# Performance work log

Measured on AMD Instinct MI355X. Metric: run time of the kernel, lower is better.

## Reference

```python
import jax, jax.numpy as jnp
import numpy as np

T = 2048        # q_len (current chunk)
P = 2048        # past KV cache length
HID = 4096      # hidden_size
H = 32          # num_attention_heads
D = HID // H    # head_dim = 128
THETA = 10000.0


def apply_rope(x, pos):
    # x: [H, T, D], pos: [T] int
    half = D // 2
    inv_freq = 1.0 / (THETA ** (jnp.arange(0, half, dtype=jnp.float32) / half))
    ang = pos.astype(jnp.float32)[:, None] * inv_freq[None, :]      # [T, D/2]
    cos = jnp.concatenate([jnp.cos(ang), jnp.cos(ang)], axis=-1)[None]  # [1, T, D]
    sin = jnp.concatenate([jnp.sin(ang), jnp.sin(ang)], axis=-1)[None]
    rot = jnp.concatenate([-x[..., half:], x[..., :half]], axis=-1)
    return x * cos + rot * sin


def setup_inputs() -> dict:
    key = jax.random.key(0)
    ks = jax.random.split(key, 8)
    s = 1.0 / np.sqrt(HID)
    inp = {
        "hidden_states": jax.random.normal(ks[0], (T, HID), dtype=jnp.float32),
        "attention_mask": jnp.triu(jnp.full((T, T), -jnp.inf, dtype=jnp.float32), k=1),
        "Wq": jax.random.normal(ks[1], (HID, HID), dtype=jnp.float32) * s,
        "Wk": jax.random.normal(ks[2], (HID, HID), dtype=jnp.float32) * s,
        "Wv": jax.random.normal(ks[3], (HID, HID), dtype=jnp.float32) * s,
        "Wo": jax.random.normal(ks[4], (HID, HID), dtype=jnp.float32) * s,
        "past_k": jax.random.normal(ks[5], (H, P, D), dtype=jnp.float32),
        "past_v": jax.random.normal(ks[6], (H, P, D), dtype=jnp.float32),
        "position_ids": P + jnp.arange(T, dtype=jnp.int32),
        "past_length": P,
    }
    return inp


def reference(hidden_states, attention_mask, Wq, Wk, Wv, Wo, past_k, past_v,
              position_ids, past_length):
    # QKV projections -> [H, T, D]
    proj = lambda W: (hidden_states @ W).reshape(T, H, D).transpose(1, 0, 2)
    q, k, v = proj(Wq), proj(Wk), proj(Wv)
    q = apply_rope(q, position_ids)
    k = apply_rope(k, position_ids)

    scale = 1.0 / jnp.sqrt(jnp.float32(D))
    # scores against past cache and current chunk (fp32 softmax, as in source)
    past_dots = (jnp.einsum('htd,hsd->hts', q, past_k) * scale).astype(jnp.float32)
    pmask = jnp.where(jnp.arange(P) < past_length, 0.0, -jnp.inf)  # [P]
    past_dots = past_dots + pmask
    cur = ((jnp.einsum('htd,hsd->hts', q, k) * scale) + attention_mask).astype(jnp.float32)

    # online-softmax merge via logsumexp combination
    past_lse = jax.scipy.special.logsumexp(past_dots, axis=-1, keepdims=True)
    cur_lse = jax.scipy.special.logsumexp(cur, axis=-1, keepdims=True)
    tot_lse = jnp.logaddexp(past_lse, cur_lse)
    pw = jnp.exp(past_dots - tot_lse).astype(q.dtype)
    cw = jnp.exp(cur - tot_lse).astype(q.dtype)

    out = jnp.einsum('hts,hsd->htd', pw, past_v) + jnp.einsum('hts,hsd->htd', cw, v)
    out = jnp.where(past_length == 0,
                    jnp.einsum('hts,hsd->htd', jax.nn.softmax(cur, axis=-1).astype(q.dtype), v),
                    out)
    out = out.transpose(1, 0, 2).reshape(T, HID)   # [T, hidden]
    return out @ Wo
```

## Files before the change

kernel.cpp:

```cpp
#include <hip/hip_runtime.h>
#include <cstdint>
#include <cstddef>

#define T_LEN 2048
#define PAST_MAX 2048
#define HID 4096
#define NHEAD 32
#define DHEAD 128

typedef __bf16 bf16_t;
typedef __bf16 bf16x4 __attribute__((ext_vector_type(4)));
typedef __bf16 bf16x8 __attribute__((ext_vector_type(8)));
typedef float  f32x4  __attribute__((ext_vector_type(4)));
typedef float  f32x16 __attribute__((ext_vector_type(16)));
typedef unsigned int u32x4 __attribute__((ext_vector_type(4)));

__device__ __forceinline__ void gload16(const void* g, void* l){
  __builtin_amdgcn_global_load_lds((const __attribute__((address_space(1))) void*)g,
                                   (__attribute__((address_space(3))) void*)l,
                                   16, 0, 0);
}

__device__ __forceinline__ unsigned pack_bf16(float a, float b){
  const unsigned ua = __builtin_bit_cast(unsigned short, (bf16_t)a);
  const unsigned ub = __builtin_bit_cast(unsigned short, (bf16_t)b);
  return ua | (ub << 16);
}

__global__ void cvt2_k(const float* __restrict__ a, bf16_t* __restrict__ ao,
                       const float* __restrict__ b, bf16_t* __restrict__ bo, int n4){
  int i = blockIdx.x * 256 + threadIdx.x;
  if (i < n4){
    const float4 v = ((const float4*)a)[i];
    bf16x4 o = { (bf16_t)v.x, (bf16_t)v.y, (bf16_t)v.z, (bf16_t)v.w };
    ((bf16x4*)ao)[i] = o;
  } else {
    i -= n4;
    const float4 v = ((const float4*)b)[i];
    bf16x4 o = { (bf16_t)v.x, (bf16_t)v.y, (bf16_t)v.z, (bf16_t)v.w };
    ((bf16x4*)bo)[i] = o;
  }
}

__global__ __launch_bounds__(256) void transpose2_k(const float* __restrict__ in,
                                                    bf16_t* __restrict__ out, int R, int C){
  __shared__ float tile[64][65];
  const int r0 = blockIdx.x << 6, c0 = blockIdx.y << 6;
  const size_t bo = (size_t)blockIdx.z * (size_t)R * (size_t)C;
  const int tx = threadIdx.x & 15, ty = threadIdx.x >> 4;
#pragma unroll
  for (int k = 0; k < 4; ++k){
    const float4 v = *(const float4*)(in + bo + (size_t)(r0 + ty + 16*k) * C + c0 + tx*4);
    float* tp = &tile[ty + 16*k][tx*4];
    tp[0] = v.x; tp[1] = v.y; tp[2] = v.z; tp[3] = v.w;
  }
  __syncthreads();
  const int rr0 = (threadIdx.x & 7) * 8;
  const int ccb = threadIdx.x >> 3;
#pragma unroll
  for (int k = 0; k < 2; ++k){
    const int cc = ccb + 32*k;
    bf16x8 o;
#pragma unroll
    for (int j = 0; j < 8; ++j) o[j] = (bf16_t)tile[rr0 + j][cc];
    *(bf16x8*)(out + bo + (size_t)(c0 + cc) * R + r0 + rr0) = o;
  }
}

__global__ __launch_bounds__(256) void transpose3_k(
    const float* __restrict__ s0, const float* __restrict__ s1, const float* __restrict__ s2,
    bf16_t* __restrict__ d0, bf16_t* __restrict__ d1, bf16_t* __restrict__ d2){
  __shared__ float tile[64][65];
  const float* in = (blockIdx.z == 0) ? s0 : (blockIdx.z == 1) ? s1 : s2;
  bf16_t* out = (blockIdx.z == 0) ? d0 : (blockIdx.z == 1) ? d1 : d2;
  const int r0 = blockIdx.x << 6, c0 = blockIdx.y << 6;
  const int tx = threadIdx.x & 15, ty = threadIdx.x >> 4;
#pragma unroll
  for (int k = 0; k < 4; ++k){
    const float4 v = *(const float4*)(in + (size_t)(r0 + ty + 16*k) * HID + c0 + tx*4);
    float* tp = &tile[ty + 16*k][tx*4];
    tp[0] = v.x; tp[1] = v.y; tp[2] = v.z; tp[3] = v.w;
  }
  __syncthreads();
  const int rr0 = (threadIdx.x & 7) * 8;
  const int ccb = threadIdx.x >> 3;
#pragma unroll
  for (int k = 0; k < 2; ++k){
    const int cc = ccb + 32*k;
    bf16x8 o;
#pragma unroll
    for (int j = 0; j < 8; ++j) o[j] = (bf16_t)tile[rr0 + j][cc];
    *(bf16x8*)(out + (size_t)(c0 + cc) * HID + r0 + rr0) = o;
  }
}

__global__ void ropek_k(bf16_t* __restrict__ K, const int* __restrict__ pos){
  const int idx = blockIdx.x * 256 + threadIdx.x;
  const int i = idx & 63;
  const int t = (idx >> 6) & (T_LEN - 1);
  const int h = idx >> 17;
  const size_t base = ((size_t)h * T_LEN + t) * DHEAD;
  const float p = (float)pos[t];
  const float inv = __expf(-(float)i * 0.14391156605212898f);
  const float ang = p * inv;
  float sn, cs;
  sincosf(ang, &sn, &cs);
  const float b0 = (float)K[base + i], b1 = (float)K[base + i + 64];
  K[base + i]      = (bf16_t)(b0 * cs - b1 * sn);
  K[base + i + 64] = (bf16_t)(b1 * cs + b0 * sn);
}

__global__ __launch_bounds__(512, 1) void gemmqkv8p_k(
    const bf16_t* __restrict__ A,
    const bf16_t* __restrict__ B0, const bf16_t* __restrict__ B1, const bf16_t* __restrict__ B2,
    bf16_t* __restrict__ OQ, bf16_t* __restrict__ OK2, bf16_t* __restrict__ OVT, int cpx)
{
  const int bid = blockIdx.x;
  const int wg  = (bid & 7) * cpx + (bid >> 3);
  const int mt  = wg & 7;
  const int nt  = wg >> 3;
  const int z   = nt >> 4;
  const int m0  = mt << 8;
  const int n0  = (nt & 15) << 8;
  const bf16_t* __restrict__ B = (z == 0) ? B0 : (z == 1) ? B1 : B2;

  const int tid = threadIdx.x;
  const int wv = tid >> 6, lane = tid & 63, lm = lane & 15, g = lane >> 4;
  const int wr = wv >> 2, wc = wv & 3;

  __shared__ __align__(16) char smem[131072];

  const f32x4 fzero = {0.f, 0.f, 0.f, 0.f};
  f32x4 acc[8][4];
#pragma unroll
  for (int i = 0; i < 8; ++i)
#pragma unroll
    for (int j = 0; j < 4; ++j) acc[i][j] = fzero;

  size_t soff[2];
#pragma unroll
  for (int i = 0; i < 2; ++i){
    const int c = i * 512 + tid;
    const int d = c >> 3, cc = c & 7;
    soff[i] = (size_t)(2 * d + (cc >> 2)) * HID + (size_t)((((cc & 3) ^ (d & 3)) << 3));
  }
  const bf16_t* Abase = A + (size_t)m0 * HID;
  const bf16_t* Bbase = B + (size_t)n0 * HID;
  const int ldst0 = ((0 * 512 + wv * 64) << 4);
  const int ldst1 = ((1 * 512 + wv * 64) << 4);

  auto stgA = [&](int kt){
    char* tb = smem + (kt & 3) * 32768;
    const bf16_t* src = Abase + (size_t)kt * 32;
    gload16(src + soff[0], tb + ldst0);
    gload16(src + soff[1], tb + ldst1);
  };
  auto stgB = [&](int kt){
    char* tb = smem + (kt & 3) * 32768 + 16384;
    const bf16_t* src = Bbase + (size_t)kt * 32;
    gload16(src + soff[0], tb + ldst0);
    gload16(src + soff[1], tb + ldst1);
  };

  const int fsw = (((g ^ ((lm >> 1) & 3)) << 4)) + ((lm & 1) << 6) + ((lm >> 1) << 7);
  const int aB_ = (wr << 13) + fsw;
  const int bB_ = 16384 + (wc << 12) + fsw;

  stgA(0); stgB(0); stgA(1); stgB(1); stgA(2); stgB(2);
  asm volatile("s_waitcnt vmcnt(8)" ::: "memory");
  __builtin_amdgcn_s_barrier();

  for (int kt = 0; kt < 128; ++kt){
    const char* tb = smem + (kt & 3) * 32768;

    bf16x8 bfr[4], afr[4];
#pragma unroll
    for (int ni = 0; ni < 4; ++ni) bfr[ni] = *(const bf16x8*)(tb + bB_ + ni * 1024);
#pragma unroll
    for (int mf = 0; mf < 4; ++mf) afr[mf] = *(const bf16x8*)(tb + aB_ + mf * 1024);
    if (kt < 125) stgA(kt + 3);
    __builtin_amdgcn_s_barrier();
    asm volatile("s_waitcnt lgkmcnt(0)" ::: "memory");
    __builtin_amdgcn_s_setprio(1);
#pragma unroll
    for (int mf = 0; mf < 4; ++mf)
#pragma unroll
      for (int ni = 0; ni < 4; ++ni)
        acc[mf][ni] = __builtin_amdgcn_mfma_f32_16x16x32_bf16(afr[mf], bfr[ni], acc[mf][ni], 0, 0, 0);
    __builtin_amdgcn_s_setprio(0);

    bf16x8 afr2[4];
#pragma unroll
    for (int mf = 0; mf < 4; ++mf) afr2[mf] = *(const bf16x8*)(tb + aB_ + (mf + 4) * 1024);
    if (kt < 125) stgB(kt + 3);
    asm volatile("s_waitcnt lgkmcnt(0)" ::: "memory");
    if (kt < 125)       asm volatile("s_waitcnt vmcnt(8)" ::: "memory");
    else if (kt == 125) asm volatile("s_waitcnt vmcnt(4)" ::: "memory");
    else                asm volatile("s_waitcnt vmcnt(0)" ::: "memory");
    __builtin_amdgcn_s_barrier();
    __builtin_amdgcn_s_setprio(1);
#pragma unroll
    for (int mf = 0; mf < 4; ++mf)
#pragma unroll
      for (int ni = 0; ni < 4; ++ni)
        acc[mf + 4][ni] = __builtin_amdgcn_mfma_f32_16x16x32_bf16(afr2[mf], bfr[ni], acc[mf + 4][ni], 0, 0, 0);
    __builtin_amdgcn_s_setprio(0);
  }

#pragma unroll
  for (int ni = 0; ni < 4; ++ni){
    const int col = n0 + wc * 64 + ni * 16 + lm;
    const int hh = col >> 7, dd = col & 127;
#pragma unroll
    for (int mf = 0; mf < 8; ++mf)
#pragma unroll
      for (int r = 0; r < 4; ++r){
        const int trow = m0 + wr * 128 + mf * 16 + g * 4 + r;
        const bf16_t v = (bf16_t)acc[mf][ni][r];
        if (z == 2)      OVT[((size_t)hh * DHEAD + dd) * T_LEN + trow] = v;
        else if (z == 1) OK2[((size_t)hh * T_LEN + trow) * DHEAD + dd] = v;
        else             OQ [((size_t)hh * T_LEN + trow) * DHEAD + dd] = v;
      }
  }
}

__global__ __launch_bounds__(512, 1) void gemm4p_k(
    const bf16_t* __restrict__ A, const bf16_t* __restrict__ B,
    float* __restrict__ OF, int cpx)
{
  const int bid = blockIdx.x;
  const int wg  = (bid & 7) * cpx + (bid >> 3);
  const int mt  = wg & 7;
  const int nt  = wg >> 3;
  const int m0  = mt << 8;
  const int n0  = nt << 7;

  const int tid = threadIdx.x;
  const int wv = tid >> 6, lane = tid & 63, lm = lane & 15, g = lane >> 4;
  const int wr = wv >> 1, wc = wv & 1;

  __shared__ __align__(16) char smem[98304];

  const f32x4 fzero = {0.f, 0.f, 0.f, 0.f};
  f32x4 acc[4][4];
#pragma unroll
  for (int i = 0; i < 4; ++i)
#pragma unroll
    for (int j = 0; j < 4; ++j) acc[i][j] = fzero;

  int srow[2], schk[2];
#pragma unroll
  for (int i = 0; i < 2; ++i){
    const int c = i * 512 + tid;
    srow[i] = c >> 3;
    schk[i] = (c & 7) ^ (srow[i] & 7);
  }
  const int sdst0 = ((0 * 512 + wv * 64) << 4);
  const int sdst1 = ((1 * 512 + wv * 64) << 4);

  auto stg = [&](int kt, int op){
    if (kt < 64){
      char* dst = smem + (kt & 1) * 49152 + op * 16384;
      const bf16_t* base = (op < 2) ? A + (size_t)(m0 + (op << 7)) * HID
                                    : B + (size_t)n0 * HID;
      base += kt * 64;
      gload16(base + (size_t)srow[0] * HID + schk[0] * 8, dst + sdst0);
      gload16(base + (size_t)srow[1] * HID + schk[1] * 8, dst + sdst1);
    }
  };

  const int koff0 = ((g)     ^ (lm & 7)) << 4;
  const int koff1 = ((4 + g) ^ (lm & 7)) << 4;
  const int abase = ((wr >> 1) << 14) + ((((wr & 1) << 6) + lm) << 7);
  const int bbase = 32768 + ((((wc << 6)) + lm) << 7);

  bf16x8 bfr[4][2];
  auto dsB = [&](int buf){
    const char* p = smem + buf * 49152 + bbase;
#pragma unroll
    for (int ni = 0; ni < 4; ++ni){
      bfr[ni][0] = *(const bf16x8*)(p + ni * 2048 + koff0);
      bfr[ni][1] = *(const bf16x8*)(p + ni * 2048 + koff1);
    }
  };

  stg(0, 2);
  stg(0, 0); stg(0, 1);
  stg(1, 2);
  asm volatile("s_waitcnt vmcnt(2)" ::: "memory");
  __builtin_amdgcn_s_barrier();

  for (int t = 0; t < 32; ++t){
    const int c0 = 2 * t, c1 = 2 * t + 1;
    const bool last = (t == 31);

#pragma unroll
    for (int half = 0; half < 2; ++half){
      const char* bufp = smem + half * 49152;
      bf16x8 afr[2][2];
      dsB(half);
#pragma unroll
      for (int mf = 0; mf < 2; ++mf){
        afr[mf][0] = *(const bf16x8*)(bufp + abase + mf * 2048 + koff0);
        afr[mf][1] = *(const bf16x8*)(bufp + abase + mf * 2048 + koff1);
      }
      if (half == 0){ stg(c1, 0); stg(c1, 1); }
      else          { stg(c0 + 2, 0); stg(c0 + 2, 1); }
      __builtin_amdgcn_s_barrier();
      asm volatile("s_waitcnt lgkmcnt(0)" ::: "memory");
      __builtin_amdgcn_s_setprio(1);
#pragma unroll
      for (int kk = 0; kk < 2; ++kk)
#pragma unroll
        for (int mf = 0; mf < 2; ++mf)
#pragma unroll
          for (int ni = 0; ni < 4; ++ni)
            acc[mf][ni] = __builtin_amdgcn_mfma_f32_16x16x32_bf16(afr[mf][kk], bfr[ni][kk], acc[mf][ni], 0, 0, 0);
      __builtin_amdgcn_s_setprio(0);
      __builtin_amdgcn_s_barrier();

#pragma unroll
      for (int mf = 0; mf < 2; ++mf){
        afr[mf][0] = *(const bf16x8*)(bufp + abase + (mf + 2) * 2048 + koff0);
        afr[mf][1] = *(const bf16x8*)(bufp + abase + (mf + 2) * 2048 + koff1);
      }
      if (half == 0) stg(c0 + 2, 2);
      else           stg(c1 + 2, 2);
      if (last) asm volatile("s_waitcnt vmcnt(0)" ::: "memory");
      else      asm volatile("s_waitcnt vmcnt(2)" ::: "memory");
      __builtin_amdgcn_s_barrier();
      asm volatile("s_waitcnt lgkmcnt(0)" ::: "memory");
      __builtin_amdgcn_s_setprio(1);
#pragma unroll
      for (int kk = 0; kk < 2; ++kk)
#pragma unroll
        for (int mf = 0; mf < 2; ++mf)
#pragma unroll
          for (int ni = 0; ni < 4; ++ni)
            acc[mf + 2][ni] = __builtin_amdgcn_mfma_f32_16x16x32_bf16(afr[mf][kk], bfr[ni][kk], acc[mf + 2][ni], 0, 0, 0);
      __builtin_amdgcn_s_setprio(0);
      __builtin_amdgcn_s_barrier();
    }
  }

#pragma unroll
  for (int ni = 0; ni < 4; ++ni){
    const int col = n0 + wc * 64 + ni * 16 + lm;
#pragma unroll
    for (int mf = 0; mf < 4; ++mf)
#pragma unroll
      for (int r = 0; r < 4; ++r){
        const int trow = m0 + wr * 64 + mf * 16 + g * 4 + r;
        OF[(size_t)trow * HID + col] = acc[mf][ni][r];
      }
  }
}

__global__ __launch_bounds__(256, 2) void attn2_k(
    const bf16_t* __restrict__ Q,
    const bf16_t* __restrict__ Kc,
    const bf16_t* __restrict__ VTc,
    const bf16_t* __restrict__ Kp,
    const bf16_t* __restrict__ VTp,
    bf16_t* __restrict__ Ctx,
    const int* __restrict__ plen_p,
    const int* __restrict__ pos)
{
  const int bid = blockIdx.x;
  const int xcd = bid & 7;
  const int k   = bid >> 3;
  const int ho  = k >> 4;
  const int qraw= k & 15;
  const int h   = (xcd << 2) | ho;
  const int qb  = (ho & 2) ? (15 - qraw) : qraw;

  const int tid = threadIdx.x;
  const int w = tid >> 6, lane = tid & 63, l31 = lane & 31, hi = lane >> 5;
  const int qw0 = qb * 128 + w * 32;
  const int qrow = qw0 + l31;
  const int plen = plen_p[0];
  const int npast = (plen + 63) >> 6;
  const int NT = npast + 2 * qb + 2;

  __shared__ __align__(16) char smem[65536 + 512];
  float* lred = (float*)(smem + 65536);

  const bf16_t* qbase = Q + ((size_t)h * T_LEN + qrow) * DHEAD;
  bf16x8 qf[8];
#pragma unroll
  for (int dc = 0; dc < 8; ++dc)
    qf[dc] = *(const bf16x8*)(qbase + dc * 16 + 8 * hi);
  {
    const float ppos = (float)pos[qrow];
    const float qs = 0.08838834764831845f;
#pragma unroll
    for (int dc = 0; dc < 4; ++dc)
#pragma unroll
      for (int j = 0; j < 8; ++j){
        const int fi = dc * 16 + 8 * hi + j;
        const float invf = __expf(-(float)fi * 0.14391156605212898f);
        float sn, cs;
        sincosf(ppos * invf, &sn, &cs);
        const float a0 = (float)qf[dc][j], a1 = (float)qf[dc + 4][j];
        qf[dc][j]     = (bf16_t)((a0 * cs - a1 * sn) * qs);
        qf[dc + 4][j] = (bf16_t)((a1 * cs + a0 * sn) * qs);
      }
  }
  __builtin_amdgcn_sched_barrier(0);

  const f32x16 fz = {0.f,0.f,0.f,0.f,0.f,0.f,0.f,0.f,0.f,0.f,0.f,0.f,0.f,0.f,0.f,0.f};
  f32x16 o[4] = {fz, fz, fz, fz};
  float m = -1e30f, l = 0.f;

  auto stage = [&](int t, int buf){
    const bf16_t* kb; const bf16_t* vb;
    if (t < npast){
      const int s0 = t * 64;
      kb = Kp  + ((size_t)h * PAST_MAX + s0) * DHEAD;
      vb = VTp + (size_t)h * DHEAD * PAST_MAX + s0;
    } else {
      const int s0 = (t - npast) * 64;
      kb = Kc  + ((size_t)h * T_LEN + s0) * DHEAD;
      vb = VTc + (size_t)h * DHEAD * T_LEN + s0;
    }
    char* kl = smem + buf * 32768;
    char* vl = kl + 16384;
#pragma unroll
    for (int i = 0; i < 4; ++i){
      const int c = i * 256 + w * 64 + lane;
      const int krow = c >> 4, kcol = c & 15;
      gload16(kb + (size_t)krow * DHEAD + ((kcol ^ (krow & 7)) << 3), kl + (i * 256 + w * 64) * 16);
      const int vrow = c >> 3, vcol = c & 7;
      gload16(vb + (size_t)vrow * 2048 + ((vcol ^ (vrow & 7)) << 3), vl + (i * 256 + w * 64) * 16);
    }
  };

  stage(0, 0);
  __builtin_amdgcn_sched_barrier(0);

  for (int t = 0; t < NT; ++t){
    const int cur = t & 1;
    if (t + 1 < NT){
      stage(t + 1, cur ^ 1);
      asm volatile("s_waitcnt vmcnt(8)" ::: "memory");
    } else {
      asm volatile("s_waitcnt vmcnt(0)" ::: "memory");
    }
    __builtin_amdgcn_sched_barrier(0);
    __builtin_amdgcn_s_barrier();
    __builtin_amdgcn_sched_barrier(0);

    const bool isc = (t >= npast);
    const int s0c = (t - npast) * 64;
    const bool active = !isc || (s0c <= qw0 + 31);

    if (active){
      char* kl = smem + cur * 32768;
      char* vl = kl + 16384;

      f32x16 sacc[2] = {fz, fz};
      __builtin_amdgcn_s_setprio(1);
#pragma unroll
      for (int kvh = 0; kvh < 2; ++kvh){
        const int krow = (kvh << 5) + l31;
        const int kbo = krow << 8;
        const int sw = (krow & 7) << 4;
#pragma unroll
        for (int dc = 0; dc < 8; ++dc){
          const bf16x8 kf = *(const bf16x8*)(kl + kbo + ((dc * 32 + 16 * hi) ^ sw));
          sacc[kvh] = __builtin_amdgcn_mfma_f32_32x32x16_bf16(kf, qf[dc], sacc[kvh], 0, 0, 0);
        }
      }
      __builtin_amdgcn_s_setprio(0);

      const bool mcur  = isc && (s0c + 63 > qw0);
      const bool mpast = !isc && ((t + 1) * 64 > plen);
      float pv[2][16];
      float pm = -1e30f;
      if (mcur | mpast){
#pragma unroll
        for (int kvh = 0; kvh < 2; ++kvh)
#pragma unroll
          for (int r = 0; r < 16; ++r){
            float x = sacc[kvh][r];
            const int kvoff = (kvh << 5) + (r & 3) + 8 * (r >> 2) + 4 * hi;
            if (mcur  && (s0c + kvoff >  qrow)) x = -1e30f;
            if (mpast && (t * 64 + kvoff >= plen)) x = -1e30f;
            pv[kvh][r] = x;
            pm = fmaxf(pm, x);
          }
      } else {
#pragma unroll
        for (int kvh = 0; kvh < 2; ++kvh)
#pragma unroll
          for (int r = 0; r < 16; ++r){
            pv[kvh][r] = sacc[kvh][r];
            pm = fmaxf(pm, sacc[kvh][r]);
          }
      }
      pm = fmaxf(pm, __shfl_xor(pm, 32));

      if (!__all(pm - m <= 8.f)){
        const float mn = fmaxf(m, pm);
        const float corr = __expf(m - mn);
        m = mn;
        l *= corr;
        if (hi == 0) lred[(w << 5) + l31] = corr;
        asm volatile("s_waitcnt lgkmcnt(0)" ::: "memory");
#pragma unroll
        for (int r = 0; r < 16; ++r){
          const float cc = lred[(w << 5) + (r & 3) + 8 * (r >> 2) + 4 * hi];
#pragma unroll
          for (int nb = 0; nb < 4; ++nb) o[nb][r] *= cc;
        }
      }

      float sum = 0.f;
#pragma unroll
      for (int kvh = 0; kvh < 2; ++kvh)
#pragma unroll
        for (int r = 0; r < 16; ++r){
          const float pe = __expf(pv[kvh][r] - m);
          pv[kvh][r] = pe;
          sum += pe;
        }
      sum += __shfl_xor(sum, 32);
      l += sum;

      unsigned wds[2][8];
#pragma unroll
      for (int kvh = 0; kvh < 2; ++kvh)
#pragma unroll
        for (int i = 0; i < 8; ++i)
          wds[kvh][i] = pack_bf16(pv[kvh][2 * i], pv[kvh][2 * i + 1]);

      bf16x8 pf[4];
#pragma unroll
      for (int ks = 0; ks < 4; ++ks){
        const int s = ks & 1, kvh = ks >> 1;
        const unsigned a0 = hi ? wds[kvh][4 * s]     : wds[kvh][4 * s + 2];
        const unsigned a1 = hi ? wds[kvh][4 * s + 1] : wds[kvh][4 * s + 3];
        const unsigned z0 = (unsigned)__shfl_xor((int)a0, 32);
        const unsigned z1 = (unsigned)__shfl_xor((int)a1, 32);
        u32x4 fw;
        fw[0] = hi ? z0 : wds[kvh][4 * s];
        fw[1] = hi ? z1 : wds[kvh][4 * s + 1];
        fw[2] = hi ? wds[kvh][4 * s + 2] : z0;
        fw[3] = hi ? wds[kvh][4 * s + 3] : z1;
        pf[ks] = __builtin_bit_cast(bf16x8, fw);
      }

      __builtin_amdgcn_s_setprio(1);
#pragma unroll
      for (int ks = 0; ks < 4; ++ks)
#pragma unroll
        for (int nb = 0; nb < 4; ++nb){
          const int vrow = (nb << 5) + l31;
          const bf16x8 vf = *(const bf16x8*)(vl + (vrow << 7) + ((ks * 32 + 16 * hi) ^ ((vrow & 7) << 4)));
          o[nb] = __builtin_amdgcn_mfma_f32_32x32x16_bf16(pf[ks], vf, o[nb], 0, 0, 0);
        }
      __builtin_amdgcn_s_setprio(0);
    }
    __builtin_amdgcn_sched_barrier(0);
    __builtin_amdgcn_s_barrier();
  }

  if (hi == 0) lred[(w << 5) + l31] = l;
  asm volatile("s_waitcnt lgkmcnt(0)" ::: "memory");
#pragma unroll
  for (int r = 0; r < 16; ++r){
    const int cr = (r & 3) + 8 * (r >> 2) + 4 * hi;
    const float li = 1.f / lred[(w << 5) + cr];
    const int trow = qw0 + cr;
    bf16_t* cb = Ctx + (size_t)trow * HID + h * DHEAD + l31;
#pragma unroll
    for (int nb = 0; nb < 4; ++nb)
      cb[nb << 5] = (bf16_t)(o[nb][r] * li);
  }
}

extern "C" void kernel_launch(void* const* d_in, const int* in_sizes, int n_in,
                              void* d_out, int out_size, void* d_ws, size_t ws_size,
                              hipStream_t stream)
{
  const float* X   = (const float*)d_in[0];
  const float* Wq  = (const float*)d_in[2];
  const float* Wk  = (const float*)d_in[3];
  const float* Wv  = (const float*)d_in[4];
  const float* Wo  = (const float*)d_in[5];
  const float* PKi = (const float*)d_in[6];
  const float* PVi = (const float*)d_in[7];
  const int* POS   = (const int*)d_in[8];
  const int* PLEN  = (const int*)d_in[9];
  float* OUT = (float*)d_out;

  char* ws = (char*)d_ws;
  const size_t SZ_XB  = (size_t)T_LEN * HID * 2;
  const size_t SZ_W   = (size_t)HID * HID * 2;
  const size_t SZ_HTD = (size_t)NHEAD * T_LEN * DHEAD * 2;

  bf16_t* XB  = (bf16_t*)(ws);
  bf16_t* WT0 = (bf16_t*)(ws + SZ_XB);
  bf16_t* WT1 = (bf16_t*)(ws + SZ_XB + SZ_W);
  bf16_t* WT2 = (bf16_t*)(ws + SZ_XB + 2 * SZ_W);
  char* p = ws + SZ_XB + 3 * SZ_W;
  bf16_t* QB   = (bf16_t*)p; p += SZ_HTD;
  bf16_t* KB   = (bf16_t*)p; p += SZ_HTD;
  bf16_t* VTB  = (bf16_t*)p; p += SZ_HTD;
  bf16_t* KPB  = (bf16_t*)p; p += SZ_HTD;
  bf16_t* VPTB = (bf16_t*)p; p += SZ_HTD;
  bf16_t* CTX  = (bf16_t*)p; p += SZ_HTD;
  bf16_t* WOT  = QB;

  dim3 blk256(256);
  dim3 blk512(512);
  cvt2_k<<<16384, blk256, 0, stream>>>(X, XB, PKi, KPB, T_LEN * HID / 4);
  transpose3_k<<<dim3(64,64,3), blk256, 0, stream>>>(Wq, Wk, Wv, WT0, WT1, WT2);
  transpose2_k<<<dim3(32,2,32), blk256, 0, stream>>>(PVi, VPTB, PAST_MAX, DHEAD);

  gemmqkv8p_k<<<384, blk512, 0, stream>>>(XB, WT0, WT1, WT2, QB, KB, VTB, 48);
  ropek_k<<<16384, blk256, 0, stream>>>(KB, POS);
  attn2_k<<<512, blk256, 0, stream>>>(QB, KB, VTB, KPB, VPTB, CTX, PLEN, POS);

  transpose2_k<<<dim3(64,64,1), blk256, 0, stream>>>(Wo, WOT, HID, HID);
  gemm4p_k<<<256, blk512, 0, stream>>>(CTX, WOT, OUT, 32);
}
```

Measured before the change: 604.3 us.

## Restructure QKV GEMM main loop into four-quadrant ping-pong with K=64 stages

Rewrites the fused QKV GEMM's inner loop to use BK=64 double-buffered LDS tiles split into A/B halves. Compute is issued as four 16-MFMA quadrants, each interleaved with a load of the next half-tile. The LDS swizzle becomes an XOR over 8 chunks, and the V-transposed epilogue writes 4 bf16 values per vector store. The aim is to halve the loop iteration count, overlap global-to-LDS loads with MFMA work more finely, and cut scattered stores. In exchange there are more barriers per iteration and the quadrant staging order is more fragile.

```diff
diff --git a/kernel.cpp b/kernel.cpp
--- a/kernel.cpp
+++ b/kernel.cpp
@@ -110,9 +110,23 @@
   K[base + i + 64] = (bf16_t)(b1 * cs + b0 * sn);
 }
 
-__global__ __launch_bounds__(512, 1) void gemmqkv8p_k(
+#define QUAD16(AH, NH, BF) \
+  __builtin_amdgcn_s_setprio(1); \
+  _Pragma("unroll") \
+  for (int kk = 0; kk < 2; ++kk){ \
+    _Pragma("unroll") \
+    for (int mf = 0; mf < 4; ++mf){ \
+      _Pragma("unroll") \
+      for (int ni = 0; ni < 2; ++ni) \
+        acc[(AH)*4 + mf][(NH)*2 + ni] = __builtin_amdgcn_mfma_f32_16x16x32_bf16( \
+            af[mf][kk], BF[ni][kk], acc[(AH)*4 + mf][(NH)*2 + ni], 0, 0, 0); \
+    } \
+  } \
+  __builtin_amdgcn_s_setprio(0);
+
+__global__ __launch_bounds__(512, 1) void gemmqkv8_k(
     const bf16_t* __restrict__ A,
-    const bf16_t* __restrict__ B0, const bf16_t* __restrict__ B1, const bf16_t* __restrict__ B2,
+    const bf16_t* __restrict__ B0p, const bf16_t* __restrict__ B1p, const bf16_t* __restrict__ B2p,
     bf16_t* __restrict__ OQ, bf16_t* __restrict__ OK2, bf16_t* __restrict__ OVT, int cpx)
 {
   const int bid = blockIdx.x;
@@ -122,7 +136,7 @@
   const int z   = nt >> 4;
   const int m0  = mt << 8;
   const int n0  = (nt & 15) << 8;
-  const bf16_t* __restrict__ B = (z == 0) ? B0 : (z == 1) ? B1 : B2;
+  const bf16_t* __restrict__ B = (z == 0) ? B0p : (z == 1) ? B1p : B2p;
 
   const int tid = threadIdx.x;
   const int wv = tid >> 6, lane = tid & 63, lm = lane & 15, g = lane >> 4;
@@ -137,90 +151,122 @@
 #pragma unroll
     for (int j = 0; j < 4; ++j) acc[i][j] = fzero;
 
-  size_t soff[2];
+  int arow_[2], brow_[2], jcol_[2];
 #pragma unroll
   for (int i = 0; i < 2; ++i){
-    const int c = i * 512 + tid;
-    const int d = c >> 3, cc = c & 7;
-    soff[i] = (size_t)(2 * d + (cc >> 2)) * HID + (size_t)((((cc & 3) ^ (d & 3)) << 3));
-  }
-  const bf16_t* Abase = A + (size_t)m0 * HID;
-  const bf16_t* Bbase = B + (size_t)n0 * HID;
+    const int c  = i * 512 + tid;
+    const int rl = c >> 3;
+    const int j  = (c & 7) ^ (rl & 7);
+    arow_[i] = m0 + ((rl >> 6) << 7) + (rl & 63);
+    brow_[i] = n0 + ((rl >> 5) << 6) + (rl & 31);
+    jcol_[i] = j << 3;
+  }
   const int ldst0 = ((0 * 512 + wv * 64) << 4);
   const int ldst1 = ((1 * 512 + wv * 64) << 4);
 
-  auto stgA = [&](int kt){
-    char* tb = smem + (kt & 3) * 32768;
-    const bf16_t* src = Abase + (size_t)kt * 32;
-    gload16(src + soff[0], tb + ldst0);
-    gload16(src + soff[1], tb + ldst1);
+  auto stgA = [&](int kt, int ah){
+    if ((unsigned)kt < 64u){
+      char* dst = smem + (kt & 1) * 65536 + ah * 16384;
+      const bf16_t* base = A + (size_t)kt * 64;
+      gload16(base + (size_t)(arow_[0] + ah * 64) * HID + jcol_[0], dst + ldst0);
+      gload16(base + (size_t)(arow_[1] + ah * 64) * HID + jcol_[1], dst + ldst1);
+    }
   };
-  auto stgB = [&](int kt){
-    char* tb = smem + (kt & 3) * 32768 + 16384;
-    const bf16_t* src = Bbase + (size_t)kt * 32;
-    gload16(src + soff[0], tb + ldst0);
-    gload16(src + soff[1], tb + ldst1);
+  auto stgB = [&](int kt, int nh){
+    if ((unsigned)kt < 64u){
+      char* dst = smem + (kt & 1) * 65536 + 32768 + nh * 16384;
+      const bf16_t* base = B + (size_t)kt * 64;
+      gload16(base + (size_t)(brow_[0] + nh * 32) * HID + jcol_[0], dst + ldst0);
+      gload16(base + (size_t)(brow_[1] + nh * 32) * HID + jcol_[1], dst + ldst1);
+    }
   };
 
-  const int fsw = (((g ^ ((lm >> 1) & 3)) << 4)) + ((lm & 1) << 6) + ((lm >> 1) << 7);
-  const int aB_ = (wr << 13) + fsw;
-  const int bB_ = 16384 + (wc << 12) + fsw;
-
-  stgA(0); stgB(0); stgA(1); stgB(1); stgA(2); stgB(2);
-  asm volatile("s_waitcnt vmcnt(8)" ::: "memory");
+  const int koff0 = ((0 + g) ^ (lm & 7)) << 4;
+  const int koff1 = ((4 + g) ^ (lm & 7)) << 4;
+  const int abase = ((wr << 6) + lm) << 7;
+  const int bbase = ((wc << 5) + lm) << 7;
+
+  stgA(0, 0); stgB(0, 0); stgB(0, 1); stgA(0, 1);
+  stgA(1, 0); stgB(1, 0); stgB(1, 1);
+  asm volatile("s_waitcnt vmcnt(6)" ::: "memory");
   __builtin_amdgcn_s_barrier();
 
-  for (int kt = 0; kt < 128; ++kt){
-    const char* tb = smem + (kt & 3) * 32768;
-
-    bf16x8 bfr[4], afr[4];
-#pragma unroll
-    for (int ni = 0; ni < 4; ++ni) bfr[ni] = *(const bf16x8*)(tb + bB_ + ni * 1024);
-#pragma unroll
-    for (int mf = 0; mf < 4; ++mf) afr[mf] = *(const bf16x8*)(tb + aB_ + mf * 1024);
-    if (kt < 125) stgA(kt + 3);
+  bf16x8 af[4][2], b0f[2][2], b1f[2][2];
+
+  for (int kt = 0; kt < 64; ++kt){
+    char* buf = smem + (kt & 1) * 65536;
+
+#pragma unroll
+    for (int mf = 0; mf < 4; ++mf){
+      af[mf][0] = *(const bf16x8*)(buf + abase + mf * 2048 + koff0);
+      af[mf][1] = *(const bf16x8*)(buf + abase + mf * 2048 + koff1);
+    }
+#pragma unroll
+    for (int ni = 0; ni < 2; ++ni){
+      b0f[ni][0] = *(const bf16x8*)(buf + 32768 + bbase + ni * 2048 + koff0);
+      b0f[ni][1] = *(const bf16x8*)(buf + 32768 + bbase + ni * 2048 + koff1);
+    }
+    stgA(kt + 1, 1);
+    __builtin_amdgcn_sched_barrier(0);
     __builtin_amdgcn_s_barrier();
     asm volatile("s_waitcnt lgkmcnt(0)" ::: "memory");
-    __builtin_amdgcn_s_setprio(1);
-#pragma unroll
-    for (int mf = 0; mf < 4; ++mf)
-#pragma unroll
-      for (int ni = 0; ni < 4; ++ni)
-        acc[mf][ni] = __builtin_amdgcn_mfma_f32_16x16x32_bf16(afr[mf], bfr[ni], acc[mf][ni], 0, 0, 0);
-    __builtin_amdgcn_s_setprio(0);
-
-    bf16x8 afr2[4];
-#pragma unroll
-    for (int mf = 0; mf < 4; ++mf) afr2[mf] = *(const bf16x8*)(tb + aB_ + (mf + 4) * 1024);
-    if (kt < 125) stgB(kt + 3);
+    __builtin_amdgcn_sched_barrier(0);
+    QUAD16(0, 0, b0f)
+    __builtin_amdgcn_s_barrier();
+
+#pragma unroll
+    for (int ni = 0; ni < 2; ++ni){
+      b1f[ni][0] = *(const bf16x8*)(buf + 49152 + bbase + ni * 2048 + koff0);
+      b1f[ni][1] = *(const bf16x8*)(buf + 49152 + bbase + ni * 2048 + koff1);
+    }
+    stgA(kt + 2, 0);
+    __builtin_amdgcn_sched_barrier(0);
+    __builtin_amdgcn_s_barrier();
     asm volatile("s_waitcnt lgkmcnt(0)" ::: "memory");
-    if (kt < 125)       asm volatile("s_waitcnt vmcnt(8)" ::: "memory");
-    else if (kt == 125) asm volatile("s_waitcnt vmcnt(4)" ::: "memory");
-    else                asm volatile("s_waitcnt vmcnt(0)" ::: "memory");
-    __builtin_amdgcn_s_barrier();
-    __builtin_amdgcn_s_setprio(1);
-#pragma unroll
-    for (int mf = 0; mf < 4; ++mf)
-#pragma unroll
-      for (int ni = 0; ni < 4; ++ni)
-        acc[mf + 4][ni] = __builtin_amdgcn_mfma_f32_16x16x32_bf16(afr2[mf], bfr[ni], acc[mf + 4][ni], 0, 0, 0);
-    __builtin_amdgcn_s_setprio(0);
-  }
-
-#pragma unroll
-  for (int ni = 0; ni < 4; ++ni){
-    const int col = n0 + wc * 64 + ni * 16 + lm;
+    __builtin_amdgcn_sched_barrier(0);
+    QUAD16(0, 1, b1f)
+    __builtin_amdgcn_s_barrier();
+
+#pragma unroll
+    for (int mf = 0; mf < 4; ++mf){
+      af[mf][0] = *(const bf16x8*)(buf + 16384 + abase + mf * 2048 + koff0);
+      af[mf][1] = *(const bf16x8*)(buf + 16384 + abase + mf * 2048 + koff1);
+    }
+    stgB(kt + 2, 0);
+    __builtin_amdgcn_sched_barrier(0);
+    __builtin_amdgcn_s_barrier();
+    asm volatile("s_waitcnt lgkmcnt(0)" ::: "memory");
+    __builtin_amdgcn_sched_barrier(0);
+    QUAD16(1, 1, b1f)
+    __builtin_amdgcn_s_barrier();
+
+    stgB(kt + 2, 1);
+    if (kt < 60) asm volatile("s_waitcnt vmcnt(6)" ::: "memory");
+    else         asm volatile("s_waitcnt vmcnt(0)" ::: "memory");
+    __builtin_amdgcn_sched_barrier(0);
+    __builtin_amdgcn_s_barrier();
+    QUAD16(1, 0, b0f)
+    __builtin_amdgcn_s_barrier();
+  }
+
+#pragma unroll
+  for (int ni4 = 0; ni4 < 4; ++ni4){
+    const int col = n0 + wc * 64 + (ni4 >> 1) * 32 + (ni4 & 1) * 16 + lm;
     const int hh = col >> 7, dd = col & 127;
 #pragma unroll
-    for (int mf = 0; mf < 8; ++mf)
-#pragma unroll
-      for (int r = 0; r < 4; ++r){
-        const int trow = m0 + wr * 128 + mf * 16 + g * 4 + r;
-        const bf16_t v = (bf16_t)acc[mf][ni][r];
-        if (z == 2)      OVT[((size_t)hh * DHEAD + dd) * T_LEN + trow] = v;
-        else if (z == 1) OK2[((size_t)hh * T_LEN + trow) * DHEAD + dd] = v;
-        else             OQ [((size_t)hh * T_LEN + trow) * DHEAD + dd] = v;
-      }
+    for (int mf8 = 0; mf8 < 8; ++mf8){
+      const int trow0 = m0 + wr * 128 + (mf8 >> 2) * 64 + (mf8 & 3) * 16 + g * 4;
+      if (z == 2){
+        bf16x4 v4 = { (bf16_t)acc[mf8][ni4][0], (bf16_t)acc[mf8][ni4][1],
+                      (bf16_t)acc[mf8][ni4][2], (bf16_t)acc[mf8][ni4][3] };
+        *(bf16x4*)(OVT + ((size_t)hh * DHEAD + dd) * T_LEN + trow0) = v4;
+      } else {
+        bf16_t* ob = (z == 1) ? OK2 : OQ;
+#pragma unroll
+        for (int r = 0; r < 4; ++r)
+          ob[((size_t)hh * T_LEN + trow0 + r) * DHEAD + dd] = (bf16_t)acc[mf8][ni4][r];
+      }
+    }
   }
 }
 
@@ -618,7 +664,7 @@
   transpose3_k<<<dim3(64,64,3), blk256, 0, stream>>>(Wq, Wk, Wv, WT0, WT1, WT2);
   transpose2_k<<<dim3(32,2,32), blk256, 0, stream>>>(PVi, VPTB, PAST_MAX, DHEAD);
 
-  gemmqkv8p_k<<<384, blk512, 0, stream>>>(XB, WT0, WT1, WT2, QB, KB, VTB, 48);
+  gemmqkv8_k<<<384, blk512, 0, stream>>>(XB, WT0, WT1, WT2, QB, KB, VTB, 48);
   ropek_k<<<16384, blk256, 0, stream>>>(KB, POS);
   attn2_k<<<512, blk256, 0, stream>>>(QB, KB, VTB, KPB, VPTB, CTX, PLEN, POS);
 
```

After: 562.8 us. -6.9%, faster.
